# Kernel optimization log

Hardware: AMD Instinct MI355X
Metric: run time of the kernel (lower is better)

## Reference

```python
import jax, jax.numpy as jnp
import numpy as np

N_NODES = 50000


def _gine(x, src, dst, edge_embed, lin_w, lin_b, nn_w, nn_b):
    # PyG GINEConv (eps=0): out = nn(x + sum_{j->i} ReLU(x_j + lin(edge_attr)))
    e = edge_embed @ lin_w + lin_b              # [E, d_in]
    msg = jax.nn.relu(x[src] + e)               # gather + fuse, [E, d_in]
    agg = jax.ops.segment_sum(msg, dst, num_segments=N_NODES)  # scatter-add, [N, d_in]
    return (x + agg) @ nn_w + nn_b              # small MLP, [N, d_out]


def setup_inputs() -> dict:
    key = jax.random.key(0)
    ks = jax.random.split(key, 20)
    E = 800000
    h = 128
    sc = lambda f_in: 1.0 / np.sqrt(f_in)
    inp = {
        "x": jax.random.normal(ks[0], (N_NODES, 1), jnp.float32),
        "edge_index": jax.random.randint(ks[1], (2, E), 0, N_NODES, jnp.int64),
        "edge_attr": jax.random.normal(ks[2], (E, 1), jnp.float32),
        "em_w": jax.random.normal(ks[3], (1, h), jnp.float32) * sc(1),
        "em_b": jnp.zeros((h,), jnp.float32),
        "l1_w": jax.random.normal(ks[4], (h, 1), jnp.float32) * sc(h),
        "l1_b": jnp.zeros((1,), jnp.float32),
        "n1_w": jax.random.normal(ks[5], (1, h), jnp.float32) * sc(1),
        "n1_b": jnp.zeros((h,), jnp.float32),
        "l2_w": jax.random.normal(ks[6], (h, h), jnp.float32) * sc(h),
        "l2_b": jnp.zeros((h,), jnp.float32),
        "n2_w": jax.random.normal(ks[7], (h, h), jnp.float32) * sc(h),
        "n2_b": jnp.zeros((h,), jnp.float32),
        "l3_w": jax.random.normal(ks[8], (h, h), jnp.float32) * sc(h),
        "l3_b": jnp.zeros((h,), jnp.float32),
        "n3_w": jax.random.normal(ks[9], (h, h), jnp.float32) * sc(h),
        "n3_b": jnp.zeros((h,), jnp.float32),
        "dec_w": jax.random.normal(ks[10], (2 * h, 1), jnp.float32) * sc(2 * h),
        "dec_b": jnp.zeros((1,), jnp.float32),
    }
    return inp


def reference(x, edge_index, edge_attr, em_w, em_b, l1_w, l1_b, n1_w, n1_b,
              l2_w, l2_b, n2_w, n2_b, l3_w, l3_b, n3_w, n3_b, dec_w, dec_b):
    src, dst = edge_index[0], edge_index[1]
    edge_embed = edge_attr @ em_w + em_b                      # [E, 128]
    hdn = _gine(x,   src, dst, edge_embed, l1_w, l1_b, n1_w, n1_b)
    hdn = _gine(hdn, src, dst, edge_embed, l2_w, l2_b, n2_w, n2_b)
    hdn = _gine(hdn, src, dst, edge_embed, l3_w, l3_b, n3_w, n3_b)
    h_cat = jnp.concatenate([hdn[src], hdn[dst]], axis=-1)    # [E, 256]
    return h_cat @ dec_w + dec_b                              # [E, 1]
```

## Files before the change

### kernel.cpp

```cpp
#include <hip/hip_runtime.h>

#define H 128
#define CAPC 3072


typedef unsigned long long ull;
using bf16x8 = __attribute__((ext_vector_type(8))) short;
using f32x4  = __attribute__((ext_vector_type(4))) float;

__device__ __forceinline__ float bf2f(unsigned short v) {
  return __uint_as_float(((unsigned)v) << 16);
}
__device__ __forceinline__ unsigned short bf16r(float v) {
  unsigned u = __float_as_uint(v);
  u = (u + 0x7FFFu + ((u >> 16) & 1u)) >> 16;
  return (unsigned short)u;
}
__device__ __forceinline__ unsigned bf16pair(float a, float b) {
  return (unsigned)bf16r(a) | ((unsigned)bf16r(b) << 16);
}

__global__ __launch_bounds__(256) void init_consts(
    const float* __restrict__ em_w, const float* __restrict__ em_b,
    const float* __restrict__ l1_w, const float* __restrict__ l1_b,
    const float* __restrict__ l2_w, const float* __restrict__ l2_b,
    const float* __restrict__ n1_b,
    const float* __restrict__ l3_w, const float* __restrict__ l3_b,
    const float* __restrict__ n2w, const float* __restrict__ n3w,
    const float* __restrict__ n3b, const float* __restrict__ dec_w,
    float* __restrict__ consts, int* __restrict__ cursor,
    unsigned short* __restrict__ w2t) {
  if (blockIdx.x > 0) {
    const int i = (blockIdx.x - 1) * 256 + threadIdx.x;
    if (i < H * H) {
      const int j = i >> 7, k = i & (H - 1);
      w2t[k * H + j] = bf16r(n2w[i]);
    }
    return;
  }
  const int k = threadIdx.x;
  cursor[k] = 0;
  cursor[k + 256] = 0;
  __shared__ float sa[H], sc[H];
  if (k < H) {
    float u2 = 0.f, c2 = 0.f, u3 = 0.f, c3 = 0.f, vA = 0.f, vB = 0.f;
    for (int j = 0; j < H; ++j) {
      const float ew = em_w[j], eb = em_b[j];
      u2 = fmaf(ew, l2_w[j * H + k], u2);
      c2 = fmaf(eb, l2_w[j * H + k], c2);
      u3 = fmaf(ew, l3_w[j * H + k], u3);
      c3 = fmaf(eb, l3_w[j * H + k], c3);
      vA = fmaf(n3w[k * H + j], dec_w[j], vA);
      vB = fmaf(n3w[k * H + j], dec_w[H + j], vB);
    }
    consts[2 + k]         = u2;
    consts[2 + H + k]     = c2 + l2_b[k] + n1_b[k];
    consts[2 + 2 * H + k] = u3;
    consts[2 + 3 * H + k] = c3 + l3_b[k];
    consts[514 + k]       = vA;
    consts[642 + k]       = vB;
    sa[k] = em_w[k] * l1_w[k];
    sc[k] = em_b[k] * l1_w[k];
  }
  __syncthreads();
  for (int s = 64; s > 0; s >>= 1) {
    if (k < s) { sa[k] += sa[k + s]; sc[k] += sc[k + s]; }
    __syncthreads();
  }
  if (k == 0) { consts[0] = sa[0]; consts[1] = sc[0] + l1_b[0]; }
  __syncthreads();
  if (k < H) {
    sa[k] = n3b[k] * dec_w[k];
    sc[k] = n3b[k] * dec_w[H + k];
  }
  __syncthreads();
  for (int s = 64; s > 0; s >>= 1) {
    if (k < s) { sa[k] += sa[k + s]; sc[k] += sc[k + s]; }
    __syncthreads();
  }
  if (k == 0) { consts[770] = sa[0]; consts[771] = sc[0]; }
}

__global__ __launch_bounds__(1024) void bin_scatter(
    const int* __restrict__ src, const int* __restrict__ dst,
    const float* __restrict__ ea, int* __restrict__ cursor,
    ull* __restrict__ spc, int E, int NBUCK) {
  __shared__ int lhist[512];
  __shared__ int lbase[512];
  const int tid = threadIdx.x;
  const int base = blockIdx.x * 2048 + tid * 2;
  if (tid < 512) lhist[tid] = 0;
  __syncthreads();
  int s_[2], d_[2], b_[2], r_[2];
  float a_[2];
#pragma unroll
  for (int j = 0; j < 2; ++j) {
    const int e = base + j;
    if (e < E) {
      s_[j] = src[e]; d_[j] = dst[e]; a_[j] = ea[e];
      b_[j] = d_[j] >> 7;
      r_[j] = atomicAdd(&lhist[b_[j]], 1);
    } else {
      b_[j] = -1;
    }
  }
  __syncthreads();
  if (tid < NBUCK && lhist[tid] > 0)
    lbase[tid] = atomicAdd(&cursor[tid], lhist[tid]);
  __syncthreads();
#pragma unroll
  for (int j = 0; j < 2; ++j) {
    if (b_[j] >= 0) {
      const int pl = lbase[b_[j]] + r_[j];
      if (pl < CAPC)
        spc[(size_t)b_[j] * CAPC + pl] =
            ((ull)(unsigned)(s_[j] | ((d_[j] & 127) << 16)) << 32) |
            (ull)(unsigned)__float_as_uint(a_[j]);
    }
  }
}

__global__ __launch_bounds__(1024) void fine_scatter(
    const int* __restrict__ cursor, const ull* __restrict__ spc,
    const float* __restrict__ x, const float* __restrict__ consts,
    int2* __restrict__ spf, int* __restrict__ rowstart,
    float* __restrict__ s1, int N) {
  __shared__ int lh[128];
  __shared__ int sd[128];
  __shared__ int cur[128];
  __shared__ int2 pay[CAPC];
  const int tid = threadIdx.x;
  const int b = blockIdx.x;
  const int cnt = min(cursor[b], CAPC);
  const size_t rbase = (size_t)b * CAPC;
  if (tid < 128) lh[tid] = 0;
  __syncthreads();
  for (int i = tid; i < cnt; i += 1024)
    atomicAdd(&lh[(int)((spc[rbase + i] >> 48) & 127u)], 1);
  __syncthreads();
  if (tid < 128) sd[tid] = lh[tid];
  __syncthreads();
  for (int off = 1; off < 128; off <<= 1) {
    int t = 0;
    if (tid < 128 && tid >= off) t = sd[tid - off];
    __syncthreads();
    if (tid < 128) sd[tid] += t;
    __syncthreads();
  }
  if (tid < 128) {
    const int ex = sd[tid] - lh[tid];
    cur[tid] = ex;
    rowstart[b * 129 + tid] = (int)rbase + ex;
    if (tid == 0) rowstart[b * 129 + 128] = (int)rbase + cnt;
  }
  __syncthreads();
  for (int i = tid; i < cnt; i += 1024) {
    const ull payv = spc[rbase + i];
    const int dl = (int)((payv >> 48) & 127u);
    const int pos = atomicAdd(&cur[dl], 1);
    pay[pos] = make_int2((int)((payv >> 32) & 0xFFFFu), (int)(unsigned)payv);
  }
  __syncthreads();
  for (int i = tid; i < cnt; i += 1024) spf[rbase + i] = pay[i];
  const int lane = tid & 63, w = tid >> 6;
  const float a1 = consts[0], c1 = consts[1];
  for (int i = w; i < 128; i += 16) {
    const int n = (b << 7) + i;
    if (n >= N) break;
    const int rsl = sd[i] - lh[i], ci = lh[i];
    float part = 0.f;
    for (int j = lane; j < ci; j += 64) {
      const int2 pv = pay[rsl + j];
      part += fmaxf(x[pv.x] + fmaf(a1, __int_as_float(pv.y), c1), 0.f);
    }
#pragma unroll
    for (int o = 32; o >= 1; o >>= 1) part += __shfl_xor(part, o, 64);
    if (lane == 0) s1[n] = x[n] + part;
  }
}

__global__ __launch_bounds__(1024) void layer2_fused(
    const int* __restrict__ rowstart, const int2* __restrict__ sp,
    const float* __restrict__ s1, const float* __restrict__ n1w,
    const float* __restrict__ n1b, const float* __restrict__ consts,
    const unsigned short* __restrict__ w2t, const float* __restrict__ n2b,
    unsigned short* __restrict__ h2b, int N) {
  __shared__ unsigned short t2s[16][136];
  __shared__ unsigned short hs[16][128];
  const int tid = threadIdx.x, w = tid >> 6, lane = tid & 63;
  const int node0 = blockIdx.x * 16;
  {
    const int n = node0 + w;
    if (n < N) {
      const int rb = (n >> 7) * 129 + (n & 127);
      const int rs = rowstart[rb], re = rowstart[rb + 1];
      const float w0 = n1w[lane],            w1 = n1w[lane + 64];
      const float u0 = consts[2 + lane],     u1 = consts[2 + lane + 64];
      const float c0 = consts[2 + H + lane], c1 = consts[2 + H + lane + 64];
      float acc0 = 0.f, acc1 = 0.f;
      for (int base = rs; base < re; base += 64) {
        const int i = base + lane;
        float s1v = 0.f, eav = 0.f;
        if (i < re) {
          const int2 sv = sp[i];
          s1v = s1[sv.x];
          eav = __int_as_float(sv.y);
        }
        const int cntv = min(64, re - base);
        for (int j = 0; j < cntv; ++j) {
          const float s = __shfl(s1v, j, 64);
          const float a = __shfl(eav, j, 64);
          acc0 += fmaxf(fmaf(s, w0, fmaf(a, u0, c0)), 0.f);
          acc1 += fmaxf(fmaf(s, w1, fmaf(a, u1, c1)), 0.f);
        }
      }
      const float sn = s1[n];
      t2s[w][lane]      = bf16r(fmaf(sn, w0, n1b[lane])      + acc0);
      t2s[w][lane + 64] = bf16r(fmaf(sn, w1, n1b[lane + 64]) + acc1);
    } else {
      t2s[w][lane] = 0;
      t2s[w][lane + 64] = 0;
    }
  }
  __syncthreads();
  if (w < 8) {
    const int t = w, col = lane & 15, quad = lane >> 4;
    const bf16x8 a0 = *(const bf16x8*)&t2s[col][quad * 8];
    const bf16x8 a1 = *(const bf16x8*)&t2s[col][32 + quad * 8];
    const bf16x8 a2 = *(const bf16x8*)&t2s[col][64 + quad * 8];
    const bf16x8 a3 = *(const bf16x8*)&t2s[col][96 + quad * 8];
    const bf16x8* bcol =
        (const bf16x8*)(w2t + (size_t)(t * 16 + col) * H + quad * 8);
    f32x4 acc = {0.f, 0.f, 0.f, 0.f};
    acc = __builtin_amdgcn_mfma_f32_16x16x32_bf16(a0, bcol[0], acc, 0, 0, 0);
    acc = __builtin_amdgcn_mfma_f32_16x16x32_bf16(a1, bcol[4], acc, 0, 0, 0);
    acc = __builtin_amdgcn_mfma_f32_16x16x32_bf16(a2, bcol[8], acc, 0, 0, 0);
    acc = __builtin_amdgcn_mfma_f32_16x16x32_bf16(a3, bcol[12], acc, 0, 0, 0);
    const float bias = n2b[t * 16 + col];
#pragma unroll
    for (int r = 0; r < 4; ++r)
      hs[quad * 4 + r][t * 16 + col] = bf16r(acc[r] + bias);
  }
  __syncthreads();
  const int row = tid >> 6, word = tid & 63;
  ((unsigned*)h2b)[(size_t)(node0 + row) * 64 + word] =
      ((const unsigned*)hs)[row * 64 + word];
}

__global__ __launch_bounds__(256) void layer3_dot(
    const int* __restrict__ rowstart, const int2* __restrict__ sp,
    const unsigned short* __restrict__ h2b, const float* __restrict__ consts,
    float* __restrict__ p, float* __restrict__ q, int N) {
  const int n = (blockIdx.x * blockDim.x + threadIdx.x) >> 6;
  const int lane = threadIdx.x & 63;
  if (n >= N) return;
  const int k0 = 2 * lane;
  const float u0 = consts[2 + 2 * H + k0], u1 = consts[2 + 2 * H + k0 + 1];
  const float c0 = consts[2 + 3 * H + k0], c1 = consts[2 + 3 * H + k0 + 1];
  const float vA0 = consts[514 + k0], vA1 = consts[514 + k0 + 1];
  const float vB0 = consts[642 + k0], vB1 = consts[642 + k0 + 1];
  const int rb = (n >> 7) * 129 + (n & 127);
  const int rs = rowstart[rb], re = rowstart[rb + 1];
  float acc0 = 0.f, acc1 = 0.f;
  for (int base = rs; base < re; base += 64) {
    const int i = base + lane;
    int esrc = 0;
    float eav = 0.f;
    if (i < re) {
      const int2 sv = sp[i];
      esrc = sv.x;
      eav = __int_as_float(sv.y);
    }
    const int cntv = min(64, re - base);
    int j = 0;
    for (; j + 8 <= cntv; j += 8) {
      int ss[8];
      float aa[8];
      ushort2 hh[8];
#pragma unroll
      for (int u = 0; u < 8; ++u) {
        ss[u] = __shfl(esrc, j + u, 64);
        aa[u] = __shfl(eav, j + u, 64);
      }
#pragma unroll
      for (int u = 0; u < 8; ++u)
        hh[u] = *(const ushort2*)&h2b[(size_t)ss[u] * H + k0];
#pragma unroll
      for (int u = 0; u < 8; ++u) {
        acc0 += fmaxf(bf2f(hh[u].x) + fmaf(aa[u], u0, c0), 0.f);
        acc1 += fmaxf(bf2f(hh[u].y) + fmaf(aa[u], u1, c1), 0.f);
      }
    }
    for (; j + 4 <= cntv; j += 4) {
      const int s0 = __shfl(esrc, j, 64),     s1i = __shfl(esrc, j + 1, 64);
      const int s2 = __shfl(esrc, j + 2, 64), s3 = __shfl(esrc, j + 3, 64);
      const float a0 = __shfl(eav, j, 64),     a1 = __shfl(eav, j + 1, 64);
      const float a2 = __shfl(eav, j + 2, 64), a3 = __shfl(eav, j + 3, 64);
      const ushort2 h0 = *(const ushort2*)&h2b[(size_t)s0 * H + k0];
      const ushort2 h1 = *(const ushort2*)&h2b[(size_t)s1i * H + k0];
      const ushort2 h2v = *(const ushort2*)&h2b[(size_t)s2 * H + k0];
      const ushort2 h3 = *(const ushort2*)&h2b[(size_t)s3 * H + k0];
      acc0 += fmaxf(bf2f(h0.x) + fmaf(a0, u0, c0), 0.f);
      acc1 += fmaxf(bf2f(h0.y) + fmaf(a0, u1, c1), 0.f);
      acc0 += fmaxf(bf2f(h1.x) + fmaf(a1, u0, c0), 0.f);
      acc1 += fmaxf(bf2f(h1.y) + fmaf(a1, u1, c1), 0.f);
      acc0 += fmaxf(bf2f(h2v.x) + fmaf(a2, u0, c0), 0.f);
      acc1 += fmaxf(bf2f(h2v.y) + fmaf(a2, u1, c1), 0.f);
      acc0 += fmaxf(bf2f(h3.x) + fmaf(a3, u0, c0), 0.f);
      acc1 += fmaxf(bf2f(h3.y) + fmaf(a3, u1, c1), 0.f);
    }
    for (; j < cntv; ++j) {
      const int s0 = __shfl(esrc, j, 64);
      const float a0 = __shfl(eav, j, 64);
      const ushort2 hv = *(const ushort2*)&h2b[(size_t)s0 * H + k0];
      acc0 += fmaxf(bf2f(hv.x) + fmaf(a0, u0, c0), 0.f);
      acc1 += fmaxf(bf2f(hv.y) + fmaf(a0, u1, c1), 0.f);
    }
  }
  const ushort2 hn = *(const ushort2*)&h2b[(size_t)n * H + k0];
  const float t0 = bf2f(hn.x) + acc0;
  const float t1 = bf2f(hn.y) + acc1;
  float pd = t0 * vA0 + t1 * vA1;
  float qd = t0 * vB0 + t1 * vB1;
#pragma unroll
  for (int o = 32; o >= 1; o >>= 1) {
    pd += __shfl_xor(pd, o, 64);
    qd += __shfl_xor(qd, o, 64);
  }
  if (lane == 0) {
    p[n] = pd + consts[770];
    q[n] = qd + consts[771];
  }
}

__global__ void final_kernel(const int* __restrict__ src,
                             const int* __restrict__ dst,
                             const float* __restrict__ p,
                             const float* __restrict__ q,
                             const float* __restrict__ dec_b,
                             float* __restrict__ out, int E) {
  const int e0 = (blockIdx.x * blockDim.x + threadIdx.x) * 2;
  if (e0 + 1 < E) {
    const int2 s2 = *(const int2*)&src[e0];
    const int2 d2 = *(const int2*)&dst[e0];
    const float db = dec_b[0];
    float2 o;
    o.x = p[s2.x] + q[d2.x] + db;
    o.y = p[s2.y] + q[d2.y] + db;
    *(float2*)&out[e0] = o;
  } else if (e0 < E) {
    out[e0] = p[src[e0]] + q[dst[e0]] + dec_b[0];
  }
}

extern "C" void kernel_launch(void* const* d_in, const int* in_sizes, int n_in,
                              void* d_out, int out_size, void* d_ws, size_t ws_size,
                              hipStream_t stream) {
  const float* x     = (const float*)d_in[0];
  const int*   ei    = (const int*)d_in[1];
  const float* ea    = (const float*)d_in[2];
  const float* em_w  = (const float*)d_in[3];
  const float* em_b  = (const float*)d_in[4];
  const float* l1_w  = (const float*)d_in[5];
  const float* l1_b  = (const float*)d_in[6];
  const float* n1_w  = (const float*)d_in[7];
  const float* n1_b  = (const float*)d_in[8];
  const float* l2_w  = (const float*)d_in[9];
  const float* l2_b  = (const float*)d_in[10];
  const float* n2_w  = (const float*)d_in[11];
  const float* n2_b  = (const float*)d_in[12];
  const float* l3_w  = (const float*)d_in[13];
  const float* l3_b  = (const float*)d_in[14];
  const float* n3_w  = (const float*)d_in[15];
  const float* n3_b  = (const float*)d_in[16];
  const float* dec_w = (const float*)d_in[17];
  const float* dec_b = (const float*)d_in[18];
  float* out = (float*)d_out;

  const int N = in_sizes[0];
  const int E = in_sizes[2];
  const int* src = ei;
  const int* dst = ei + E;

  const int NBUCK  = (N + 127) >> 7;
  const int NBATCH = (E + 2047) >> 11;
  const int NPAD   = ((N + 15) / 16) * 16;
  const int NT16   = NPAD / 16;

  float* ws       = (float*)d_ws;
  float* consts   = ws;
  ull*   spc      = (ull*)(ws + 1024);
  int2*  spf      = (int2*)(spc + (size_t)NBUCK * CAPC);
  unsigned short* h2b = (unsigned short*)(spf + (size_t)NBUCK * CAPC);
  unsigned short* w2t = h2b + (size_t)NPAD * H;
  float* s1       = (float*)(w2t + H * H);
  float* p        = s1 + N;
  float* q        = p + N;
  int*   cursor   = (int*)(q + N);
  int*   rowstart = cursor + 512;

  init_consts<<<65, 256, 0, stream>>>(em_w, em_b, l1_w, l1_b, l2_w, l2_b,
                                      n1_b, l3_w, l3_b, n2_w, n3_w, n3_b,
                                      dec_w, consts, cursor, w2t);
  bin_scatter<<<NBATCH, 1024, 0, stream>>>(src, dst, ea, cursor, spc, E, NBUCK);
  fine_scatter<<<NBUCK, 1024, 0, stream>>>(cursor, spc, x, consts, spf,
                                           rowstart, s1, N);
  layer2_fused<<<NT16, 1024, 0, stream>>>(rowstart, spf, s1, n1_w, n1_b,
                                          consts, w2t, n2_b, h2b, N);
  layer3_dot<<<(N + 3) / 4, 256, 0, stream>>>(rowstart, spf, h2b, consts,
                                              p, q, N);
  final_kernel<<<(E / 2 + 255) / 256, 256, 0, stream>>>(src, dst, p, q, dec_b,
                                                        out, E);
}
```

Measured before the change: 215.4 us.

## Fuse bucket sort with layer-2 aggregation and MLP; move layer-1 sum to atomics

Layer-1 neighbour sums are now added with global float atomics inside the binning pass, into a buffer zeroed by extra init_consts blocks. The fine-sort kernel and the layer-2 kernel are merged into one per-bucket kernel. It writes the sorted edges, accumulates layer-2 messages into an LDS tile using run-length segmented atomics, then runs the bf16 MFMA node MLP directly from LDS. This removes a kernel launch, a pass over the sorted edge list and the separate s1 reduction. The cost is large LDS use per block, which limits occupancy, fewer and longer-running blocks, and nondeterministic float atomic ordering.

```diff
diff --git a/kernel.cpp b/kernel.cpp
--- a/kernel.cpp
+++ b/kernel.cpp
@@ -29,7 +29,12 @@
     const float* __restrict__ n2w, const float* __restrict__ n3w,
     const float* __restrict__ n3b, const float* __restrict__ dec_w,
     float* __restrict__ consts, int* __restrict__ cursor,
-    unsigned short* __restrict__ w2t) {
+    unsigned short* __restrict__ w2t, float* __restrict__ s1acc, int N) {
+  if (blockIdx.x > 64) {
+    const int i = (blockIdx.x - 65) * 256 + threadIdx.x;
+    if (i < N) s1acc[i] = 0.f;
+    return;
+  }
   if (blockIdx.x > 0) {
     const int i = (blockIdx.x - 1) * 256 + threadIdx.x;
     if (i < H * H) {
@@ -83,14 +88,16 @@
 
 __global__ __launch_bounds__(1024) void bin_scatter(
     const int* __restrict__ src, const int* __restrict__ dst,
-    const float* __restrict__ ea, int* __restrict__ cursor,
-    ull* __restrict__ spc, int E, int NBUCK) {
+    const float* __restrict__ ea, const float* __restrict__ x,
+    const float* __restrict__ consts, float* __restrict__ s1acc,
+    int* __restrict__ cursor, ull* __restrict__ spc, int E, int NBUCK) {
   __shared__ int lhist[512];
   __shared__ int lbase[512];
   const int tid = threadIdx.x;
   const int base = blockIdx.x * 2048 + tid * 2;
   if (tid < 512) lhist[tid] = 0;
   __syncthreads();
+  const float a1 = consts[0], c1 = consts[1];
   int s_[2], d_[2], b_[2], r_[2];
   float a_[2];
 #pragma unroll
@@ -100,6 +107,7 @@
       s_[j] = src[e]; d_[j] = dst[e]; a_[j] = ea[e];
       b_[j] = d_[j] >> 7;
       r_[j] = atomicAdd(&lhist[b_[j]], 1);
+      atomicAdd(&s1acc[d_[j]], fmaxf(x[s_[j]] + fmaf(a1, a_[j], c1), 0.f));
     } else {
       b_[j] = -1;
     }
@@ -120,22 +128,28 @@
   }
 }
 
-__global__ __launch_bounds__(1024) void fine_scatter(
+__global__ __launch_bounds__(512, 4) void sort_mlp2(
     const int* __restrict__ cursor, const ull* __restrict__ spc,
-    const float* __restrict__ x, const float* __restrict__ consts,
-    int2* __restrict__ spf, int* __restrict__ rowstart,
-    float* __restrict__ s1, int N) {
+    const float* __restrict__ x, const float* __restrict__ s1acc,
+    const float* __restrict__ consts, const float* __restrict__ n1w,
+    const float* __restrict__ n1b, const unsigned short* __restrict__ w2t,
+    const float* __restrict__ n2b, int2* __restrict__ spf,
+    int* __restrict__ rowstart, unsigned short* __restrict__ h2b, int N) {
   __shared__ int lh[128];
   __shared__ int sd[128];
   __shared__ int cur[128];
-  __shared__ int2 pay[CAPC];
+  __shared__ float agg[128 * 132];
+  __shared__ float scr[8][256];
   const int tid = threadIdx.x;
   const int b = blockIdx.x;
   const int cnt = min(cursor[b], CAPC);
   const size_t rbase = (size_t)b * CAPC;
+  const int w = tid >> 6, lane = tid & 63;
+
   if (tid < 128) lh[tid] = 0;
-  __syncthreads();
-  for (int i = tid; i < cnt; i += 1024)
+  for (int idx = tid; idx < 128 * 132; idx += 512) agg[idx] = 0.f;
+  __syncthreads();
+  for (int i = tid; i < cnt; i += 512)
     atomicAdd(&lh[(int)((spc[rbase + i] >> 48) & 127u)], 1);
   __syncthreads();
   if (tid < 128) sd[tid] = lh[tid];
@@ -154,97 +168,95 @@
     if (tid == 0) rowstart[b * 129 + 128] = (int)rbase + cnt;
   }
   __syncthreads();
-  for (int i = tid; i < cnt; i += 1024) {
-    const ull payv = spc[rbase + i];
-    const int dl = (int)((payv >> 48) & 127u);
+  for (int i = tid; i < cnt; i += 512) {
+    const ull pv = spc[rbase + i];
+    const int dl = (int)((pv >> 48) & 127u);
     const int pos = atomicAdd(&cur[dl], 1);
-    pay[pos] = make_int2((int)((payv >> 32) & 0xFFFFu), (int)(unsigned)payv);
-  }
-  __syncthreads();
-  for (int i = tid; i < cnt; i += 1024) spf[rbase + i] = pay[i];
-  const int lane = tid & 63, w = tid >> 6;
-  const float a1 = consts[0], c1 = consts[1];
-  for (int i = w; i < 128; i += 16) {
-    const int n = (b << 7) + i;
-    if (n >= N) break;
-    const int rsl = sd[i] - lh[i], ci = lh[i];
-    float part = 0.f;
-    for (int j = lane; j < ci; j += 64) {
-      const int2 pv = pay[rsl + j];
-      part += fmaxf(x[pv.x] + fmaf(a1, __int_as_float(pv.y), c1), 0.f);
-    }
-#pragma unroll
-    for (int o = 32; o >= 1; o >>= 1) part += __shfl_xor(part, o, 64);
-    if (lane == 0) s1[n] = x[n] + part;
-  }
-}
-
-__global__ __launch_bounds__(1024) void layer2_fused(
-    const int* __restrict__ rowstart, const int2* __restrict__ sp,
-    const float* __restrict__ s1, const float* __restrict__ n1w,
-    const float* __restrict__ n1b, const float* __restrict__ consts,
-    const unsigned short* __restrict__ w2t, const float* __restrict__ n2b,
-    unsigned short* __restrict__ h2b, int N) {
-  __shared__ unsigned short t2s[16][136];
-  __shared__ unsigned short hs[16][128];
-  const int tid = threadIdx.x, w = tid >> 6, lane = tid & 63;
-  const int node0 = blockIdx.x * 16;
+    spf[rbase + pos] = make_int2((int)((pv >> 32) & 0xFFFFFFu), (int)(unsigned)pv);
+  }
+  __syncthreads();
   {
-    const int n = node0 + w;
-    if (n < N) {
-      const int rb = (n >> 7) * 129 + (n & 127);
-      const int rs = rowstart[rb], re = rowstart[rb + 1];
-      const float w0 = n1w[lane],            w1 = n1w[lane + 64];
-      const float u0 = consts[2 + lane],     u1 = consts[2 + lane + 64];
-      const float c0 = consts[2 + H + lane], c1 = consts[2 + H + lane + 64];
-      float acc0 = 0.f, acc1 = 0.f;
-      for (int base = rs; base < re; base += 64) {
-        const int i = base + lane;
-        float s1v = 0.f, eav = 0.f;
-        if (i < re) {
-          const int2 sv = sp[i];
-          s1v = s1[sv.x];
-          eav = __int_as_float(sv.y);
+    const float w0 = n1w[lane],               w1 = n1w[lane + 64];
+    const float u0 = consts[2 + lane],        u1 = consts[2 + lane + 64];
+    const float cc0 = consts[2 + H + lane],   cc1 = consts[2 + H + lane + 64];
+    float racc0 = 0.f, racc1 = 0.f;
+    int rdl = -1;
+    for (int base = w * 64; base < cnt; base += 512) {
+      const int i = base + lane;
+      float s1v = 0.f, eav = 0.f;
+      int dlv = 0;
+      if (i < cnt) {
+        const int2 sv = spf[rbase + i];
+        const int sx = sv.x & 0xFFFF;
+        dlv = (sv.x >> 16) & 127;
+        eav = __int_as_float(sv.y);
+        s1v = x[sx] + s1acc[sx];
+      }
+      f32x4 pk = {s1v, eav, __int_as_float(dlv), 0.f};
+      *(f32x4*)&scr[w][lane * 4] = pk;
+      const int m = min(64, cnt - base);
+      for (int j = 0; j < m; ++j) {
+        const f32x4 e = *(const f32x4*)&scr[w][j * 4];
+        const int dl = __builtin_amdgcn_readfirstlane(__float_as_int(e[2]));
+        if (dl != rdl) {
+          if (rdl >= 0) {
+            atomicAdd(&agg[rdl * 132 + lane], racc0);
+            atomicAdd(&agg[rdl * 132 + 64 + lane], racc1);
+          }
+          rdl = dl; racc0 = 0.f; racc1 = 0.f;
         }
-        const int cntv = min(64, re - base);
-        for (int j = 0; j < cntv; ++j) {
-          const float s = __shfl(s1v, j, 64);
-          const float a = __shfl(eav, j, 64);
-          acc0 += fmaxf(fmaf(s, w0, fmaf(a, u0, c0)), 0.f);
-          acc1 += fmaxf(fmaf(s, w1, fmaf(a, u1, c1)), 0.f);
-        }
+        racc0 += fmaxf(fmaf(e[0], w0, fmaf(e[1], u0, cc0)), 0.f);
+        racc1 += fmaxf(fmaf(e[0], w1, fmaf(e[1], u1, cc1)), 0.f);
       }
-      const float sn = s1[n];
-      t2s[w][lane]      = bf16r(fmaf(sn, w0, n1b[lane])      + acc0);
-      t2s[w][lane + 64] = bf16r(fmaf(sn, w1, n1b[lane + 64]) + acc1);
-    } else {
-      t2s[w][lane] = 0;
-      t2s[w][lane + 64] = 0;
-    }
-  }
-  __syncthreads();
-  if (w < 8) {
-    const int t = w, col = lane & 15, quad = lane >> 4;
-    const bf16x8 a0 = *(const bf16x8*)&t2s[col][quad * 8];
-    const bf16x8 a1 = *(const bf16x8*)&t2s[col][32 + quad * 8];
-    const bf16x8 a2 = *(const bf16x8*)&t2s[col][64 + quad * 8];
-    const bf16x8 a3 = *(const bf16x8*)&t2s[col][96 + quad * 8];
-    const bf16x8* bcol =
-        (const bf16x8*)(w2t + (size_t)(t * 16 + col) * H + quad * 8);
-    f32x4 acc = {0.f, 0.f, 0.f, 0.f};
-    acc = __builtin_amdgcn_mfma_f32_16x16x32_bf16(a0, bcol[0], acc, 0, 0, 0);
-    acc = __builtin_amdgcn_mfma_f32_16x16x32_bf16(a1, bcol[4], acc, 0, 0, 0);
-    acc = __builtin_amdgcn_mfma_f32_16x16x32_bf16(a2, bcol[8], acc, 0, 0, 0);
-    acc = __builtin_amdgcn_mfma_f32_16x16x32_bf16(a3, bcol[12], acc, 0, 0, 0);
-    const float bias = n2b[t * 16 + col];
-#pragma unroll
-    for (int r = 0; r < 4; ++r)
-      hs[quad * 4 + r][t * 16 + col] = bf16r(acc[r] + bias);
-  }
-  __syncthreads();
-  const int row = tid >> 6, word = tid & 63;
-  ((unsigned*)h2b)[(size_t)(node0 + row) * 64 + word] =
-      ((const unsigned*)hs)[row * 64 + word];
+    }
+    if (rdl >= 0) {
+      atomicAdd(&agg[rdl * 132 + lane], racc0);
+      atomicAdd(&agg[rdl * 132 + 64 + lane], racc1);
+    }
+  }
+  __syncthreads();
+  for (int idx = tid; idx < 128 * 128; idx += 512) {
+    const int node = idx >> 7, k = idx & 127;
+    const int g = (b << 7) + node;
+    if (g < N)
+      agg[node * 132 + k] += (x[g] + s1acc[g]) * n1w[k] + n1b[k];
+  }
+  __syncthreads();
+  {
+    const int nt = w;
+    const int c = lane & 15, q = lane >> 4;
+    const float* arow = &agg[(nt * 16 + c) * 132 + q * 8];
+    bf16x8 afr[4];
+#pragma unroll
+    for (int kc = 0; kc < 4; ++kc) {
+      const f32x4 f0 = *(const f32x4*)(arow + kc * 32);
+      const f32x4 f1 = *(const f32x4*)(arow + kc * 32 + 4);
+      union { bf16x8 v; unsigned u[4]; } pkk;
+      pkk.u[0] = bf16pair(f0[0], f0[1]);
+      pkk.u[1] = bf16pair(f0[2], f0[3]);
+      pkk.u[2] = bf16pair(f1[0], f1[1]);
+      pkk.u[3] = bf16pair(f1[2], f1[3]);
+      afr[kc] = pkk.v;
+    }
+    const int gbase = (b << 7) + nt * 16 + q * 4;
+#pragma unroll
+    for (int t = 0; t < 8; ++t) {
+      const bf16x8* bcol =
+          (const bf16x8*)(w2t + (size_t)(t * 16 + c) * H + q * 8);
+      f32x4 acc = {0.f, 0.f, 0.f, 0.f};
+      acc = __builtin_amdgcn_mfma_f32_16x16x32_bf16(afr[0], bcol[0], acc, 0, 0, 0);
+      acc = __builtin_amdgcn_mfma_f32_16x16x32_bf16(afr[1], bcol[4], acc, 0, 0, 0);
+      acc = __builtin_amdgcn_mfma_f32_16x16x32_bf16(afr[2], bcol[8], acc, 0, 0, 0);
+      acc = __builtin_amdgcn_mfma_f32_16x16x32_bf16(afr[3], bcol[12], acc, 0, 0, 0);
+      const float bias = n2b[t * 16 + c];
+#pragma unroll
+      for (int r = 0; r < 4; ++r) {
+        const int g = gbase + r;
+        if (g < N)
+          h2b[(size_t)g * H + t * 16 + c] = bf16r(acc[r] + bias);
+      }
+    }
+  }
 }
 
 __global__ __launch_bounds__(256) void layer3_dot(
@@ -268,7 +280,7 @@
     float eav = 0.f;
     if (i < re) {
       const int2 sv = sp[i];
-      esrc = sv.x;
+      esrc = sv.x & 0xFFFF;
       eav = __int_as_float(sv.y);
     }
     const int cntv = min(64, re - base);
@@ -385,7 +397,7 @@
   const int NBUCK  = (N + 127) >> 7;
   const int NBATCH = (E + 2047) >> 11;
   const int NPAD   = ((N + 15) / 16) * 16;
-  const int NT16   = NPAD / 16;
+  const int ZB     = (N + 255) >> 8;
 
   float* ws       = (float*)d_ws;
   float* consts   = ws;
@@ -393,20 +405,19 @@
   int2*  spf      = (int2*)(spc + (size_t)NBUCK * CAPC);
   unsigned short* h2b = (unsigned short*)(spf + (size_t)NBUCK * CAPC);
   unsigned short* w2t = h2b + (size_t)NPAD * H;
-  float* s1       = (float*)(w2t + H * H);
-  float* p        = s1 + N;
+  float* s1acc    = (float*)(w2t + H * H);
+  float* p        = s1acc + N;
   float* q        = p + N;
   int*   cursor   = (int*)(q + N);
   int*   rowstart = cursor + 512;
 
-  init_consts<<<65, 256, 0, stream>>>(em_w, em_b, l1_w, l1_b, l2_w, l2_b,
-                                      n1_b, l3_w, l3_b, n2_w, n3_w, n3_b,
-                                      dec_w, consts, cursor, w2t);
-  bin_scatter<<<NBATCH, 1024, 0, stream>>>(src, dst, ea, cursor, spc, E, NBUCK);
-  fine_scatter<<<NBUCK, 1024, 0, stream>>>(cursor, spc, x, consts, spf,
-                                           rowstart, s1, N);
-  layer2_fused<<<NT16, 1024, 0, stream>>>(rowstart, spf, s1, n1_w, n1_b,
-                                          consts, w2t, n2_b, h2b, N);
+  init_consts<<<65 + ZB, 256, 0, stream>>>(em_w, em_b, l1_w, l1_b, l2_w, l2_b,
+                                           n1_b, l3_w, l3_b, n2_w, n3_w, n3_b,
+                                           dec_w, consts, cursor, w2t, s1acc, N);
+  bin_scatter<<<NBATCH, 1024, 0, stream>>>(src, dst, ea, x, consts, s1acc,
+                                           cursor, spc, E, NBUCK);
+  sort_mlp2<<<NBUCK, 512, 0, stream>>>(cursor, spc, x, s1acc, consts, n1_w,
+                                       n1_b, w2t, n2_b, spf, rowstart, h2b, N);
   layer3_dot<<<(N + 3) / 4, 256, 0, stream>>>(rowstart, spf, h2b, consts,
                                               p, q, N);
   final_kernel<<<(E / 2 + 255) / 256, 256, 0, stream>>>(src, dst, p, q, dec_b,
```

After: 308.8 us. 1.43x slower.
